# Kernel optimization log

Hardware: AMD Instinct MI355X
Metric: run time of the kernel (lower is better)

## Reference

```python
import jax, jax.numpy as jnp
import numpy as np

B, M, D = 512, 32, 64
LAYERS = [128, 128, 128]


def _cin_layer(h, x0, W, b):
    # h: [B, H, D], x0: [B, M, D], W: [O, H*M] (1x1 conv weight squeezed), b: [O]
    O = W.shape[0]
    H = h.shape[1]
    Wr = W.reshape(O, H, M)
    # fused outer-product + 1x1 conv: z[b,h,m,d] = h[b,h,d]*x0[b,m,d]; out = W @ z
    out = jnp.einsum('bhd,bmd,ohm->bod', h, x0, Wr) + b[None, :, None]
    return jax.nn.relu(out)


def setup_inputs() -> dict:
    key = jax.random.key(0)
    ks = jax.random.split(key, 10)
    inp = {"input": jax.random.normal(ks[0], (B, M, D), dtype=jnp.float32)}
    H = M
    fan_scales = []
    Ws, bs = [], []
    for i, O in enumerate(LAYERS):
        cin = H * M
        s = 1.0 / np.sqrt(cin)
        Ws.append(jax.random.uniform(ks[1 + 2 * i], (O, cin), minval=-s, maxval=s, dtype=jnp.float32))
        bs.append(jax.random.uniform(ks[2 + 2 * i], (O,), minval=-s, maxval=s, dtype=jnp.float32))
        H = O  # direct=True
    out_dim = sum(LAYERS)
    s = 1.0 / np.sqrt(out_dim)
    inp.update({"W0": Ws[0], "b0": bs[0], "W1": Ws[1], "b1": bs[1], "W2": Ws[2], "b2": bs[2]})
    inp["lw"] = jax.random.uniform(ks[7], (1, out_dim), minval=-s, maxval=s, dtype=jnp.float32)
    inp["lb"] = jax.random.uniform(ks[8], (1,), minval=-s, maxval=s, dtype=jnp.float32)
    return inp


def reference(input, W0, b0, W1, b1, W2, b2, lw, lb):
    x0 = input  # [B, M, D]
    h = x0
    finals = []
    for W, b in ((W0, b0), (W1, b1), (W2, b2)):
        h = _cin_layer(h, x0, W, b)  # direct=True: output feeds both next hidden and final
        finals.append(h)
    result = jnp.concatenate(finals, axis=1)          # [B, sum(layers), D]
    result = jnp.sum(result, axis=-1)                  # [B, sum(layers)]
    score = result @ lw.T + lb                         # [B, 1]
    return score.squeeze(-1)                           # [B]
```

## Files before the change

kernel.cpp:

```cpp
#include <hip/hip_runtime.h>


constexpr int Bb = 512, Mm = 32, Dd = 64, Oo = 128, RES = 384;

typedef __attribute__((ext_vector_type(8))) short bf16x8;
typedef __attribute__((ext_vector_type(4))) float f32x4;

static __device__ __forceinline__ ushort f2bf(float f) {
  union { float f; uint u; } v;
  v.f = f;
  uint u = v.u;
  return (ushort)((u + 0x7FFFu + ((u >> 16) & 1u)) >> 16);
}
static __device__ __forceinline__ float bf2f(ushort b) {
  union { uint u; float f; } v;
  v.u = (uint)b << 16;
  return v.f;
}

__global__ __launch_bounds__(256) void wsplit_kernel(const float* __restrict__ W,
                                                     ushort* __restrict__ Whi,
                                                     ushort* __restrict__ Wlo, int H) {
  int t = blockIdx.x * 256 + threadIdx.x;
  if (t >= H * 8 * 64) return;
  int l = t & 63, fo = (t >> 6) & 7, hh = t >> 9;
  int o = fo * 16 + (l & 15);
  int m0 = (l >> 4) * 8;
  const float* src = W + (size_t)o * (H * 32) + hh * 32 + m0;
  ushort hi[8], lo[8];
#pragma unroll
  for (int j = 0; j < 8; ++j) {
    float w = src[j];
    ushort h = f2bf(w);
    hi[j] = h;
    lo[j] = f2bf(w - bf2f(h));
  }
  *reinterpret_cast<uint4*>(Whi + (size_t)t * 8) = *reinterpret_cast<uint4*>(hi);
  *reinterpret_cast<uint4*>(Wlo + (size_t)t * 8) = *reinterpret_cast<uint4*>(lo);
}

__global__ __launch_bounds__(256) void x0split_kernel(const float* __restrict__ x0,
                                                      ushort* __restrict__ Xhi,
                                                      ushort* __restrict__ Xlo) {
  int t = blockIdx.x * 256 + threadIdx.x;
  int l = t & 63, fd = (t >> 6) & 3, b = t >> 8;
  int d = fd * 16 + (l & 15);
  int m0 = (l >> 4) * 8;
  const float* src = x0 + ((size_t)b * Mm + m0) * Dd + d;
  ushort hi[8], lo[8];
#pragma unroll
  for (int j = 0; j < 8; ++j) {
    float w = src[j * Dd];
    ushort h = f2bf(w);
    hi[j] = h;
    lo[j] = f2bf(w - bf2f(h));
  }
  *reinterpret_cast<uint4*>(Xhi + (size_t)t * 8) = *reinterpret_cast<uint4*>(hi);
  *reinterpret_cast<uint4*>(Xlo + (size_t)t * 8) = *reinterpret_cast<uint4*>(lo);
}

template <int H>
__global__ __launch_bounds__(256, 4) void cin_mfma_kernel(
    const float* __restrict__ h_in,
    const ushort* __restrict__ Whi,
    const ushort* __restrict__ Wlo,
    const ushort* __restrict__ Xhi,
    const ushort* __restrict__ Xlo,
    const float* __restrict__ bias,
    float* __restrict__ h_out,
    float* __restrict__ res,
    int res_off) {
  __shared__ float h_lds[H * Dd];

  const int b = blockIdx.x;
  const int q = blockIdx.y;
  const int t = threadIdx.x;
  const int lane = t & 63;
  const int f = __builtin_amdgcn_readfirstlane(q * 4 + (t >> 6));
  const int cid = lane & 15;

  {
    const float4* hg = reinterpret_cast<const float4*>(h_in + (size_t)b * H * Dd);
    float4* hl = reinterpret_cast<float4*>(h_lds);
#pragma unroll
    for (int i = 0; i < H * Dd / 4 / 256; ++i) hl[t + i * 256] = hg[t + i * 256];
  }

  bf16x8 xh[4], xl[4];
#pragma unroll
  for (int fd = 0; fd < 4; ++fd) {
    size_t off = (((size_t)b * 4 + fd) * 64 + lane) * 8;
    xh[fd] = *reinterpret_cast<const bf16x8*>(Xhi + off);
    xl[fd] = *reinterpret_cast<const bf16x8*>(Xlo + off);
  }

  __syncthreads();

  const f32x4 kZ = {0.f, 0.f, 0.f, 0.f};
  f32x4 acc[4];
#pragma unroll
  for (int fd = 0; fd < 4; ++fd) acc[fd] = kZ;

  const size_t hstride = (size_t)8 * 64 * 8;
  const ushort* pwh = Whi + ((size_t)f * 64 + lane) * 8;
  const ushort* pwl = Wlo + ((size_t)f * 64 + lane) * 8;

  auto step = [&](int hh, bf16x8 ah, bf16x8 al) {
    float hv[4];
#pragma unroll
    for (int fd = 0; fd < 4; ++fd) hv[fd] = h_lds[hh * Dd + fd * 16 + cid];
    f32x4 y[4];
#pragma unroll
    for (int fd = 0; fd < 4; ++fd)
      y[fd] = __builtin_amdgcn_mfma_f32_16x16x32_bf16(ah, xh[fd], kZ, 0, 0, 0);
#pragma unroll
    for (int fd = 0; fd < 4; ++fd)
      y[fd] = __builtin_amdgcn_mfma_f32_16x16x32_bf16(ah, xl[fd], y[fd], 0, 0, 0);
#pragma unroll
    for (int fd = 0; fd < 4; ++fd)
      y[fd] = __builtin_amdgcn_mfma_f32_16x16x32_bf16(al, xh[fd], y[fd], 0, 0, 0);
#pragma unroll
    for (int fd = 0; fd < 4; ++fd)
#pragma unroll
      for (int r = 0; r < 4; ++r) acc[fd][r] = fmaf(hv[fd], y[fd][r], acc[fd][r]);
  };

  bf16x8 a0h = *reinterpret_cast<const bf16x8*>(pwh);
  bf16x8 a0l = *reinterpret_cast<const bf16x8*>(pwl);
#pragma unroll 1
  for (int hh = 0; hh < H; hh += 2) {
    bf16x8 a1h = *reinterpret_cast<const bf16x8*>(pwh + (size_t)(hh + 1) * hstride);
    bf16x8 a1l = *reinterpret_cast<const bf16x8*>(pwl + (size_t)(hh + 1) * hstride);
    step(hh, a0h, a0l);
    if (hh + 2 < H) {
      a0h = *reinterpret_cast<const bf16x8*>(pwh + (size_t)(hh + 2) * hstride);
      a0l = *reinterpret_cast<const bf16x8*>(pwl + (size_t)(hh + 2) * hstride);
    }
    step(hh + 1, a1h, a1l);
  }

  const int rg = lane >> 4;
#pragma unroll
  for (int r = 0; r < 4; ++r) {
    int o = f * 16 + rg * 4 + r;
    float bs = bias[o];
    float sd = 0.f;
#pragma unroll
    for (int fd = 0; fd < 4; ++fd) {
      float v = acc[fd][r] + bs;
      v = v > 0.f ? v : 0.f;
      if (h_out != nullptr) h_out[((size_t)b * Oo + o) * Dd + fd * 16 + cid] = v;
      sd += v;
    }
#pragma unroll
    for (int mk = 1; mk < 16; mk <<= 1) sd += __shfl_xor(sd, mk, 64);
    if (cid == 0) res[(size_t)b * RES + res_off + o] = sd;
  }
}

__global__ __launch_bounds__(64) void cin_score_kernel(
    const float* __restrict__ res, const float* __restrict__ lw,
    const float* __restrict__ lb, float* __restrict__ out) {
  const int b = blockIdx.x;
  const int lane = threadIdx.x;
  float acc = 0.f;
#pragma unroll
  for (int i = 0; i < RES / 64; ++i) {
    const int idx = i * 64 + lane;
    acc = fmaf(res[b * RES + idx], lw[idx], acc);
  }
#pragma unroll
  for (int off = 32; off >= 1; off >>= 1) acc += __shfl_xor(acc, off, 64);
  if (lane == 0) out[b] = acc + lb[0];
}

extern "C" void kernel_launch(void* const* d_in, const int* in_sizes, int n_in,
                              void* d_out, int out_size, void* d_ws, size_t ws_size,
                              hipStream_t stream) {
  const float* x0 = (const float*)d_in[0];
  const float* W0 = (const float*)d_in[1];
  const float* b0 = (const float*)d_in[2];
  const float* W1 = (const float*)d_in[3];
  const float* b1 = (const float*)d_in[4];
  const float* W2 = (const float*)d_in[5];
  const float* b2 = (const float*)d_in[6];
  const float* lw = (const float*)d_in[7];
  const float* lb = (const float*)d_in[8];
  float* out = (float*)d_out;

  float* h1 = (float*)d_ws;
  float* h2 = h1 + (size_t)Bb * Oo * Dd;
  float* res = h2 + (size_t)Bb * Oo * Dd;
  ushort* Whi0 = (ushort*)(res + (size_t)Bb * RES);
  ushort* Wlo0 = Whi0 + (size_t)32 * 8 * 64 * 8;
  ushort* Whi1 = Wlo0 + (size_t)32 * 8 * 64 * 8;
  ushort* Wlo1 = Whi1 + (size_t)128 * 8 * 64 * 8;
  ushort* Whi2 = Wlo1 + (size_t)128 * 8 * 64 * 8;
  ushort* Wlo2 = Whi2 + (size_t)128 * 8 * 64 * 8;
  ushort* Xhi = Wlo2 + (size_t)128 * 8 * 64 * 8;
  ushort* Xlo = Xhi + (size_t)Bb * 4 * 64 * 8;

  wsplit_kernel<<<dim3(64), dim3(256), 0, stream>>>(W0, Whi0, Wlo0, 32);
  wsplit_kernel<<<dim3(256), dim3(256), 0, stream>>>(W1, Whi1, Wlo1, 128);
  wsplit_kernel<<<dim3(256), dim3(256), 0, stream>>>(W2, Whi2, Wlo2, 128);
  x0split_kernel<<<dim3(512), dim3(256), 0, stream>>>(x0, Xhi, Xlo);

  cin_mfma_kernel<32><<<dim3(Bb, 2), dim3(256), 0, stream>>>(x0, Whi0, Wlo0, Xhi, Xlo, b0, h1, res, 0);
  cin_mfma_kernel<128><<<dim3(Bb, 2), dim3(256), 0, stream>>>(h1, Whi1, Wlo1, Xhi, Xlo, b1, h2, res, 128);
  cin_mfma_kernel<128><<<dim3(Bb, 2), dim3(256), 0, stream>>>(h2, Whi2, Wlo2, Xhi, Xlo, b2, nullptr, res, 256);

  cin_score_kernel<<<dim3(Bb), dim3(64), 0, stream>>>(res, lw, lb, out);
}
```

Measured before the change: 274.2 us.

## Merge prep kernels, drop LDS staging of h, software-pipeline loads

```diff
diff --git a/kernel.cpp b/kernel.cpp
--- a/kernel.cpp
+++ b/kernel.cpp
@@ -18,11 +18,10 @@
   return v.f;
 }
 
-__global__ __launch_bounds__(256) void wsplit_kernel(const float* __restrict__ W,
-                                                     ushort* __restrict__ Whi,
-                                                     ushort* __restrict__ Wlo, int H) {
-  int t = blockIdx.x * 256 + threadIdx.x;
-  if (t >= H * 8 * 64) return;
+static __device__ __forceinline__ void wsplit_one(const float* __restrict__ W,
+                                                  ushort* __restrict__ Whi,
+                                                  ushort* __restrict__ Wlo,
+                                                  int H, int t) {
   int l = t & 63, fo = (t >> 6) & 7, hh = t >> 9;
   int o = fo * 16 + (l & 15);
   int m0 = (l >> 4) * 8;
@@ -39,10 +38,9 @@
   *reinterpret_cast<uint4*>(Wlo + (size_t)t * 8) = *reinterpret_cast<uint4*>(lo);
 }
 
-__global__ __launch_bounds__(256) void x0split_kernel(const float* __restrict__ x0,
-                                                      ushort* __restrict__ Xhi,
-                                                      ushort* __restrict__ Xlo) {
-  int t = blockIdx.x * 256 + threadIdx.x;
+static __device__ __forceinline__ void x0split_one(const float* __restrict__ x0,
+                                                   ushort* __restrict__ Xhi,
+                                                   ushort* __restrict__ Xlo, int t) {
   int l = t & 63, fd = (t >> 6) & 3, b = t >> 8;
   int d = fd * 16 + (l & 15);
   int m0 = (l >> 4) * 8;
@@ -57,6 +55,25 @@
   }
   *reinterpret_cast<uint4*>(Xhi + (size_t)t * 8) = *reinterpret_cast<uint4*>(hi);
   *reinterpret_cast<uint4*>(Xlo + (size_t)t * 8) = *reinterpret_cast<uint4*>(lo);
+}
+
+__global__ __launch_bounds__(256) void prep_kernel(
+    const float* __restrict__ W0, const float* __restrict__ W1,
+    const float* __restrict__ W2, const float* __restrict__ x0,
+    ushort* __restrict__ Whi0, ushort* __restrict__ Wlo0,
+    ushort* __restrict__ Whi1, ushort* __restrict__ Wlo1,
+    ushort* __restrict__ Whi2, ushort* __restrict__ Wlo2,
+    ushort* __restrict__ Xhi, ushort* __restrict__ Xlo) {
+  int t = blockIdx.x * 256 + threadIdx.x;
+  if (t < 16384) {
+    wsplit_one(W0, Whi0, Wlo0, 32, t);
+  } else if (t < 81920) {
+    wsplit_one(W1, Whi1, Wlo1, 128, t - 16384);
+  } else if (t < 147456) {
+    wsplit_one(W2, Whi2, Wlo2, 128, t - 81920);
+  } else {
+    x0split_one(x0, Xhi, Xlo, t - 147456);
+  }
 }
 
 template <int H>
@@ -70,8 +87,6 @@
     float* __restrict__ h_out,
     float* __restrict__ res,
     int res_off) {
-  __shared__ float h_lds[H * Dd];
-
   const int b = blockIdx.x;
   const int q = blockIdx.y;
   const int t = threadIdx.x;
@@ -79,13 +94,6 @@
   const int f = __builtin_amdgcn_readfirstlane(q * 4 + (t >> 6));
   const int cid = lane & 15;
 
-  {
-    const float4* hg = reinterpret_cast<const float4*>(h_in + (size_t)b * H * Dd);
-    float4* hl = reinterpret_cast<float4*>(h_lds);
-#pragma unroll
-    for (int i = 0; i < H * Dd / 4 / 256; ++i) hl[t + i * 256] = hg[t + i * 256];
-  }
-
   bf16x8 xh[4], xl[4];
 #pragma unroll
   for (int fd = 0; fd < 4; ++fd) {
@@ -94,49 +102,75 @@
     xl[fd] = *reinterpret_cast<const bf16x8*>(Xlo + off);
   }
 
-  __syncthreads();
-
-  const f32x4 kZ = {0.f, 0.f, 0.f, 0.f};
-  f32x4 acc[4];
-#pragma unroll
-  for (int fd = 0; fd < 4; ++fd) acc[fd] = kZ;
-
+  const float* hb = h_in + (size_t)b * H * Dd + cid;
   const size_t hstride = (size_t)8 * 64 * 8;
   const ushort* pwh = Whi + ((size_t)f * 64 + lane) * 8;
   const ushort* pwl = Wlo + ((size_t)f * 64 + lane) * 8;
 
-  auto step = [&](int hh, bf16x8 ah, bf16x8 al) {
-    float hv[4];
-#pragma unroll
-    for (int fd = 0; fd < 4; ++fd) hv[fd] = h_lds[hh * Dd + fd * 16 + cid];
-    f32x4 y[4];
-#pragma unroll
-    for (int fd = 0; fd < 4; ++fd)
-      y[fd] = __builtin_amdgcn_mfma_f32_16x16x32_bf16(ah, xh[fd], kZ, 0, 0, 0);
-#pragma unroll
-    for (int fd = 0; fd < 4; ++fd)
-      y[fd] = __builtin_amdgcn_mfma_f32_16x16x32_bf16(ah, xl[fd], y[fd], 0, 0, 0);
-#pragma unroll
-    for (int fd = 0; fd < 4; ++fd)
-      y[fd] = __builtin_amdgcn_mfma_f32_16x16x32_bf16(al, xh[fd], y[fd], 0, 0, 0);
-#pragma unroll
-    for (int fd = 0; fd < 4; ++fd)
-#pragma unroll
-      for (int r = 0; r < 4; ++r) acc[fd][r] = fmaf(hv[fd], y[fd][r], acc[fd][r]);
-  };
-
-  bf16x8 a0h = *reinterpret_cast<const bf16x8*>(pwh);
-  bf16x8 a0l = *reinterpret_cast<const bf16x8*>(pwl);
+  const f32x4 kZ = {0.f, 0.f, 0.f, 0.f};
+  f32x4 acc[4];
+#pragma unroll
+  for (int fd = 0; fd < 4; ++fd) acc[fd] = kZ;
+
+  bf16x8 aAh = *reinterpret_cast<const bf16x8*>(pwh);
+  bf16x8 aAl = *reinterpret_cast<const bf16x8*>(pwl);
+  bf16x8 aBh = *reinterpret_cast<const bf16x8*>(pwh + hstride);
+  bf16x8 aBl = *reinterpret_cast<const bf16x8*>(pwl + hstride);
+  float hvA[4], hvB[4];
+#pragma unroll
+  for (int fd = 0; fd < 4; ++fd) {
+    hvA[fd] = hb[fd * 16];
+    hvB[fd] = hb[Dd + fd * 16];
+  }
+
 #pragma unroll 1
   for (int hh = 0; hh < H; hh += 2) {
-    bf16x8 a1h = *reinterpret_cast<const bf16x8*>(pwh + (size_t)(hh + 1) * hstride);
-    bf16x8 a1l = *reinterpret_cast<const bf16x8*>(pwl + (size_t)(hh + 1) * hstride);
-    step(hh, a0h, a0l);
-    if (hh + 2 < H) {
-      a0h = *reinterpret_cast<const bf16x8*>(pwh + (size_t)(hh + 2) * hstride);
-      a0l = *reinterpret_cast<const bf16x8*>(pwl + (size_t)(hh + 2) * hstride);
-    }
-    step(hh + 1, a1h, a1l);
+    const int hnA = (hh + 2 < H) ? hh + 2 : hh;
+    const int hnB = (hh + 3 < H) ? hh + 3 : hh + 1;
+
+    f32x4 y[4];
+#pragma unroll
+    for (int fd = 0; fd < 4; ++fd)
+      y[fd] = __builtin_amdgcn_mfma_f32_16x16x32_bf16(aAh, xh[fd], kZ, 0, 0, 0);
+#pragma unroll
+    for (int fd = 0; fd < 4; ++fd)
+      y[fd] = __builtin_amdgcn_mfma_f32_16x16x32_bf16(aAh, xl[fd], y[fd], 0, 0, 0);
+#pragma unroll
+    for (int fd = 0; fd < 4; ++fd)
+      y[fd] = __builtin_amdgcn_mfma_f32_16x16x32_bf16(aAl, xh[fd], y[fd], 0, 0, 0);
+    aAh = *reinterpret_cast<const bf16x8*>(pwh + (size_t)hnA * hstride);
+    aAl = *reinterpret_cast<const bf16x8*>(pwl + (size_t)hnA * hstride);
+    float nhvA[4];
+#pragma unroll
+    for (int fd = 0; fd < 4; ++fd) nhvA[fd] = hb[hnA * Dd + fd * 16];
+#pragma unroll
+    for (int fd = 0; fd < 4; ++fd)
+#pragma unroll
+      for (int r = 0; r < 4; ++r) acc[fd][r] = fmaf(hvA[fd], y[fd][r], acc[fd][r]);
+#pragma unroll
+    for (int fd = 0; fd < 4; ++fd) hvA[fd] = nhvA[fd];
+
+    f32x4 z[4];
+#pragma unroll
+    for (int fd = 0; fd < 4; ++fd)
+      z[fd] = __builtin_amdgcn_mfma_f32_16x16x32_bf16(aBh, xh[fd], kZ, 0, 0, 0);
+#pragma unroll
+    for (int fd = 0; fd < 4; ++fd)
+      z[fd] = __builtin_amdgcn_mfma_f32_16x16x32_bf16(aBh, xl[fd], z[fd], 0, 0, 0);
+#pragma unroll
+    for (int fd = 0; fd < 4; ++fd)
+      z[fd] = __builtin_amdgcn_mfma_f32_16x16x32_bf16(aBl, xh[fd], z[fd], 0, 0, 0);
+    aBh = *reinterpret_cast<const bf16x8*>(pwh + (size_t)hnB * hstride);
+    aBl = *reinterpret_cast<const bf16x8*>(pwl + (size_t)hnB * hstride);
+    float nhvB[4];
+#pragma unroll
+    for (int fd = 0; fd < 4; ++fd) nhvB[fd] = hb[hnB * Dd + fd * 16];
+#pragma unroll
+    for (int fd = 0; fd < 4; ++fd)
+#pragma unroll
+      for (int r = 0; r < 4; ++r) acc[fd][r] = fmaf(hvB[fd], z[fd][r], acc[fd][r]);
+#pragma unroll
+    for (int fd = 0; fd < 4; ++fd) hvB[fd] = nhvB[fd];
   }
 
   const int rg = lane >> 4;
@@ -200,10 +234,8 @@
   ushort* Xhi = Wlo2 + (size_t)128 * 8 * 64 * 8;
   ushort* Xlo = Xhi + (size_t)Bb * 4 * 64 * 8;
 
-  wsplit_kernel<<<dim3(64), dim3(256), 0, stream>>>(W0, Whi0, Wlo0, 32);
-  wsplit_kernel<<<dim3(256), dim3(256), 0, stream>>>(W1, Whi1, Wlo1, 128);
-  wsplit_kernel<<<dim3(256), dim3(256), 0, stream>>>(W2, Whi2, Wlo2, 128);
-  x0split_kernel<<<dim3(512), dim3(256), 0, stream>>>(x0, Xhi, Xlo);
+  prep_kernel<<<dim3(1088), dim3(256), 0, stream>>>(W0, W1, W2, x0, Whi0, Wlo0,
+                                                    Whi1, Wlo1, Whi2, Wlo2, Xhi, Xlo);
 
   cin_mfma_kernel<32><<<dim3(Bb, 2), dim3(256), 0, stream>>>(x0, Whi0, Wlo0, Xhi, Xlo, b0, h1, res, 0);
   cin_mfma_kernel<128><<<dim3(Bb, 2), dim3(256), 0, stream>>>(h1, Whi1, Wlo1, Xhi, Xlo, b1, h2, res, 128);
```

Measured after the change: 341.0 us. 1.24x slower.
